# Optimization experiments

Hardware: AMD Instinct MI355X
Metric: run time of the kernel (lower is better)

Reference implementation:

```python
import jax, jax.numpy as jnp
import numpy as np

NUM_HEADS = 16
NEG_INF = -9e15


def setup_inputs() -> dict:
    key = jax.random.key(0)
    k1, k2, k3 = jax.random.split(key, 3)
    B, S, D = 2, 2048, 1024
    # xavier-uniform-ish init scale for weights
    lim_qkv = float(np.sqrt(6.0 / (D + 3 * D)))
    lim_o = float(np.sqrt(6.0 / (D + D)))
    return {
        "x": jax.random.normal(k1, (B, S, D), dtype=jnp.float32),
        "w_qkv": jax.random.uniform(k2, (3 * D, D), minval=-lim_qkv, maxval=lim_qkv, dtype=jnp.float32),
        "b_qkv": jnp.zeros((3 * D,), dtype=jnp.float32),
        "w_o": jax.random.uniform(k3, (D, D), minval=-lim_o, maxval=lim_o, dtype=jnp.float32),
        "b_o": jnp.zeros((D,), dtype=jnp.float32),
    }


def reference(x, w_qkv, b_qkv, w_o, b_o):
    B, S, D = x.shape
    H = NUM_HEADS
    hd = D // H
    # qkv projection: [B,S,3D]
    qkv = x @ w_qkv.T + b_qkv
    # -> [B, H, S, 3*hd], then split
    qkv = qkv.reshape(B, S, H, 3 * hd).transpose(0, 2, 1, 3)
    q, k, v = jnp.split(qkv, 3, axis=-1)  # each [B,H,S,hd]
    scale = 1.0 / jnp.sqrt(jnp.asarray(hd, dtype=x.dtype))
    logits = jnp.einsum("bhqd,bhkd->bhqk", q, k) * scale
    attn = jax.nn.softmax(logits, axis=-1)
    vals = jnp.einsum("bhqk,bhkd->bhqd", attn, v)
    vals = vals.transpose(0, 2, 1, 3).reshape(B, S, D)
    return vals @ w_o.T + b_o
```

## Files before the change

kernel.cpp:

```cpp
#include <hip/hip_runtime.h>
#include <math.h>

#define NHEADS 16
#define HD 64

typedef __attribute__((ext_vector_type(8))) _Float16 half8;
typedef __attribute__((ext_vector_type(4))) _Float16 half4;
typedef __attribute__((ext_vector_type(4))) float f32x4;
typedef __attribute__((ext_vector_type(16))) float f32x16;
typedef __attribute__((ext_vector_type(4))) unsigned int u32x4;

__device__ inline void load_lds16(const void* g, void* l) {
    __builtin_amdgcn_global_load_lds(
        (const __attribute__((address_space(1))) unsigned int*)g,
        (__attribute__((address_space(3))) unsigned int*)l, 16, 0, 0);
}
__device__ inline void pl32swap(unsigned int& x, unsigned int& y) {
    asm volatile("v_permlane32_swap_b32 %0, %1" : "+v"(x), "+v"(y));
}

#define NX  4194304
#define NWQ 3145728
#define NWO 1048576
__global__ void cvt_all(const float* __restrict__ x, const float* __restrict__ wq,
                        const float* __restrict__ wo, _Float16* __restrict__ xf,
                        _Float16* __restrict__ wqf, _Float16* __restrict__ wof) {
    int i = (blockIdx.x * blockDim.x + threadIdx.x) * 8;
    const float* src; _Float16* dst; int off;
    if (i < NX)            { src = x;  dst = xf;  off = i; }
    else if (i < NX + NWQ) { src = wq; dst = wqf; off = i - NX; }
    else                   { src = wo; dst = wof; off = i - (NX + NWQ); }
    float4 a = *(const float4*)(src + off);
    float4 b = *(const float4*)(src + off + 4);
    half8 h;
    h[0] = (_Float16)a.x; h[1] = (_Float16)a.y; h[2] = (_Float16)a.z; h[3] = (_Float16)a.w;
    h[4] = (_Float16)b.x; h[5] = (_Float16)b.y; h[6] = (_Float16)b.z; h[7] = (_Float16)b.w;
    *(half8*)(dst + off) = h;
}

#define GEMM_CORE(K)                                                                   \
    __shared__ __align__(1024) unsigned char smem[16384];                              \
    const int tid = threadIdx.x;                                                       \
    const int l = tid & 63, w = tid >> 6;                                              \
    const int wr = w >> 1, wc = w & 1;                                                 \
    const int nwg = gridDim.x * gridDim.y;                                             \
    const int bid = blockIdx.y * gridDim.x + blockIdx.x;                               \
    const int swz = (bid & 7) * (nwg >> 3) + (bid >> 3);                               \
    const int m0 = (swz / gridDim.x) * 128, n0 = (swz % gridDim.x) * 128;              \
    const int srow = tid >> 2;                                                         \
    const int schunk = (tid & 3) ^ ((srow >> 1) & 3);                                  \
    const size_t gA0 = (size_t)(m0 + srow) * K + schunk * 8;                           \
    const size_t gA1 = gA0 + (size_t)64 * K;                                           \
    const size_t gB0 = (size_t)(n0 + srow) * K + schunk * 8;                           \
    const size_t gB1 = gB0 + (size_t)64 * K;                                           \
    unsigned char* ldsW = smem + w * 1024;                                             \
    const int col16 = l & 15, kc = l >> 4;                                             \
    const int ra0 = wr * 64 + col16;                                                   \
    const int offA = ra0 * 64 + ((kc ^ ((ra0 >> 1) & 3)) * 16);                        \
    const int rb0 = wc * 64 + col16;                                                   \
    const int offB = rb0 * 64 + ((kc ^ ((rb0 >> 1) & 3)) * 16);                        \
    f32x4 acc[4][4] = {};                                                              \
    for (int k0 = 0; k0 < K; k0 += 32) {                                               \
        load_lds16(A + gA0 + k0, ldsW + 0);                                            \
        load_lds16(A + gA1 + k0, ldsW + 4096);                                         \
        load_lds16(B + gB0 + k0, ldsW + 8192);                                         \
        load_lds16(B + gB1 + k0, ldsW + 12288);                                       \
        __syncthreads();                                                               \
        half8 af[4], bf[4];                                                            \
        _Pragma("unroll")                                                              \
        for (int m = 0; m < 4; ++m) af[m] = *(const half8*)(smem + offA + m * 1024);   \
        _Pragma("unroll")                                                              \
        for (int n = 0; n < 4; ++n) bf[n] = *(const half8*)(smem + 8192 + offB + n * 1024); \
        _Pragma("unroll")                                                              \
        for (int m = 0; m < 4; ++m)                                                    \
            _Pragma("unroll")                                                          \
            for (int n = 0; n < 4; ++n)                                                \
                acc[m][n] = __builtin_amdgcn_mfma_f32_16x16x32_f16(af[m], bf[n], acc[m][n], 0, 0, 0); \
        __syncthreads();                                                               \
    }

__global__ __launch_bounds__(256, 2) void gemm_o(
    const _Float16* __restrict__ A, const _Float16* __restrict__ B,
    const float* __restrict__ bias, float* __restrict__ C,
    int M, int N, int K) {
    GEMM_CORE(K)
    const int rowb = m0 + wr * 64 + (l >> 4) * 4;
    const int colb = n0 + wc * 64 + col16;
    float bv[4];
    #pragma unroll
    for (int n = 0; n < 4; ++n) bv[n] = bias[colb + n * 16];
    #pragma unroll
    for (int m = 0; m < 4; ++m)
        #pragma unroll
        for (int j = 0; j < 4; ++j) {
            float* crow = C + (size_t)(rowb + m * 16 + j) * N + colb;
            #pragma unroll
            for (int n = 0; n < 4; ++n) crow[n * 16] = acc[m][n][j] + bv[n];
        }
}

#define QSCALE 0.18033688f
__global__ __launch_bounds__(256, 2) void gemm_qkv(
    const _Float16* __restrict__ A, const _Float16* __restrict__ B,
    const float* __restrict__ bias,
    _Float16* __restrict__ Qf, _Float16* __restrict__ Kf,
    _Float16* __restrict__ VfT, int K) {
    GEMM_CORE(K)
    const int rowb = m0 + wr * 64 + (l >> 4) * 4;
    const int colb = n0 + wc * 64 + col16;
    #pragma unroll
    for (int n = 0; n < 4; ++n) {
        int col = colb + n * 16;
        int h = col / 192;
        int rem = col - h * 192;
        int part = rem >> 6, d = rem & 63;
        float bv = bias[col];
        #pragma unroll
        for (int m = 0; m < 4; ++m) {
            int r0 = rowb + m * 16;
            int b = r0 >> 11, s0r = r0 & 2047;
            int bh = b * 16 + h;
            if (part == 0) {
                #pragma unroll
                for (int j = 0; j < 4; ++j)
                    Qf[((size_t)bh * 2048 + s0r + j) * 64 + d] =
                        (_Float16)((acc[m][n][j] + bv) * QSCALE);
            } else if (part == 1) {
                #pragma unroll
                for (int j = 0; j < 4; ++j)
                    Kf[((size_t)bh * 2048 + s0r + j) * 64 + d] = (_Float16)(acc[m][n][j] + bv);
            } else {
                half4 pk;
                pk[0] = (_Float16)(acc[m][n][0] + bv);
                pk[1] = (_Float16)(acc[m][n][1] + bv);
                pk[2] = (_Float16)(acc[m][n][2] + bv);
                pk[3] = (_Float16)(acc[m][n][3] + bv);
                *(half4*)&VfT[((size_t)bh * 64 + d) * 2048 + s0r] = pk;
            }
        }
    }
}

__global__ __launch_bounds__(512, 2) void mfma_attn(
    const _Float16* __restrict__ Qf, const _Float16* __restrict__ Kf,
    const _Float16* __restrict__ VfT, _Float16* __restrict__ vals) {
    __shared__ __align__(1024) unsigned char smem[32768];
    const int tid = threadIdx.x;
    const int l = tid & 63, w = tid >> 6;
    const int l31 = l & 31, hl = l >> 5;
    const int hwbid = blockIdx.y * gridDim.x + blockIdx.x;
    const int q_t = (hwbid >> 3) & 7;
    const int bh = (hwbid & 7) + ((hwbid >> 6) << 3);
    const int q0 = q_t * 256;
    const int h = bh & 15, b = bh >> 4;

    half8 qf[4];
    {
        const _Float16* qp = Qf + ((size_t)bh * 2048 + q0 + w * 32 + l31) * 64 + hl * 8;
        #pragma unroll
        for (int c = 0; c < 4; ++c) qf[c] = *(const half8*)(qp + c * 16);
    }
    f32x16 zvec = {};
    f32x16 o0 = {}, o1 = {};
    float mshift = 0.f, lsum = 0.f;

    const _Float16* Kg = Kf + (size_t)bh * 2048 * 64;
    const _Float16* Vg = VfT + (size_t)bh * 64 * 2048;

    int offK, offV;
    {
        int row2 = w * 4 + (l >> 4);
        int slot = (l & 15) ^ (row2 & 15);
        int row = row2 * 2 + (slot >> 3);
        int chunk = slot & 7;
        offK = row * 64 + chunk * 8;
        offV = row * 2048 + chunk * 8;
    }
    const int sbase = (l31 & 1) * 8;
    const int xr = (l31 >> 1) & 15;
    const int rb0 = (l31 >> 1) * 256;

    #define STAGE(kt0, buf)                                                            \
        {                                                                              \
            unsigned char* bK = smem + (buf) * 8192 + w * 1024;                        \
            unsigned char* bV = smem + 16384 + (buf) * 8192 + w * 1024;                \
            load_lds16(Kg + (size_t)(kt0) * 64 + offK, bK);                            \
            load_lds16(Vg + (kt0) + offV, bV);                                         \
        }

    STAGE(0, 0)
    __syncthreads();
    int cur = 0;
    for (int t = 0; t < 32; ++t) {
        if (t + 1 < 32) STAGE((t + 1) * 64, cur ^ 1)
        const unsigned char* Ksb = smem + cur * 8192;
        const unsigned char* Vsb = smem + 16384 + cur * 8192;

        f32x16 s0_, s1_;
        __builtin_amdgcn_s_setprio(1);
        {
            int chOff = ((sbase + hl) ^ xr) << 4;
            half8 k0 = *(const half8*)(Ksb + rb0 + chOff);
            half8 k1 = *(const half8*)(Ksb + rb0 + 4096 + chOff);
            s0_ = __builtin_amdgcn_mfma_f32_32x32x16_f16(k0, qf[0], zvec, 0, 0, 0);
            s1_ = __builtin_amdgcn_mfma_f32_32x32x16_f16(k1, qf[0], zvec, 0, 0, 0);
        }
        #pragma unroll
        for (int kc = 1; kc < 4; ++kc) {
            int chOff = ((sbase + kc * 2 + hl) ^ xr) << 4;
            half8 k0 = *(const half8*)(Ksb + rb0 + chOff);
            half8 k1 = *(const half8*)(Ksb + rb0 + 4096 + chOff);
            s0_ = __builtin_amdgcn_mfma_f32_32x32x16_f16(k0, qf[kc], s0_, 0, 0, 0);
            s1_ = __builtin_amdgcn_mfma_f32_32x32x16_f16(k1, qf[kc], s1_, 0, 0, 0);
        }
        __builtin_amdgcn_s_setprio(0);

        if (__any(mshift != 0.f)) {
            #pragma unroll
            for (int r = 0; r < 16; ++r) { s0_[r] -= mshift; s1_[r] -= mshift; }
        }

        float r0 = 0.f, r1 = 0.f, r2 = 0.f, r3 = 0.f;
        unsigned int a[2][8];
        #pragma unroll
        for (int j = 0; j < 8; ++j) {
            float p0 = __builtin_amdgcn_exp2f(s0_[2 * j]);
            float p1 = __builtin_amdgcn_exp2f(s0_[2 * j + 1]);
            float q0_ = __builtin_amdgcn_exp2f(s1_[2 * j]);
            float q1_ = __builtin_amdgcn_exp2f(s1_[2 * j + 1]);
            r0 += p0; r1 += p1; r2 += q0_; r3 += q1_;
            a[0][j] = __builtin_bit_cast(unsigned int, __builtin_amdgcn_cvt_pkrtz(p0, p1));
            a[1][j] = __builtin_bit_cast(unsigned int, __builtin_amdgcn_cvt_pkrtz(q0_, q1_));
        }
        float rsum = (r0 + r1) + (r2 + r3);

        if (__any(rsum > 32768.f)) {
            float pmax = s0_[0];
            #pragma unroll
            for (int r = 1; r < 16; ++r) pmax = fmaxf(pmax, s0_[r]);
            #pragma unroll
            for (int r = 0; r < 16; ++r) pmax = fmaxf(pmax, s1_[r]);
            pmax = fmaxf(pmax, __shfl_xor(pmax, 32, 64));
            float d_ = fmaxf(pmax, 0.f);
            float corr = __builtin_amdgcn_exp2f(-d_);
            #pragma unroll
            for (int r = 0; r < 16; ++r) { s0_[r] -= d_; s1_[r] -= d_; }
            #pragma unroll
            for (int r = 0; r < 16; ++r) { o0[r] *= corr; o1[r] *= corr; }
            lsum *= corr;
            mshift += d_;
            r0 = r1 = r2 = r3 = 0.f;
            #pragma unroll
            for (int j = 0; j < 8; ++j) {
                float p0 = __builtin_amdgcn_exp2f(s0_[2 * j]);
                float p1 = __builtin_amdgcn_exp2f(s0_[2 * j + 1]);
                float q0_ = __builtin_amdgcn_exp2f(s1_[2 * j]);
                float q1_ = __builtin_amdgcn_exp2f(s1_[2 * j + 1]);
                r0 += p0; r1 += p1; r2 += q0_; r3 += q1_;
                a[0][j] = __builtin_bit_cast(unsigned int, __builtin_amdgcn_cvt_pkrtz(p0, p1));
                a[1][j] = __builtin_bit_cast(unsigned int, __builtin_amdgcn_cvt_pkrtz(q0_, q1_));
            }
            rsum = (r0 + r1) + (r2 + r3);
        }
        lsum += rsum;

        #pragma unroll
        for (int c = 0; c < 2; ++c) {
            pl32swap(a[c][0], a[c][2]);
            pl32swap(a[c][1], a[c][3]);
            pl32swap(a[c][4], a[c][6]);
            pl32swap(a[c][5], a[c][7]);
        }

        __builtin_amdgcn_s_setprio(1);
        #pragma unroll
        for (int kk = 0; kk < 4; ++kk) {
            u32x4 pw;
            pw.x = a[kk >> 1][(kk & 1) * 4 + 0];
            pw.y = a[kk >> 1][(kk & 1) * 4 + 1];
            pw.z = a[kk >> 1][(kk & 1) * 4 + 2];
            pw.w = a[kk >> 1][(kk & 1) * 4 + 3];
            half8 pf = __builtin_bit_cast(half8, pw);
            int chOff = ((sbase + kk * 2 + hl) ^ xr) << 4;
            half8 v0 = *(const half8*)(Vsb + rb0 + chOff);
            half8 v1 = *(const half8*)(Vsb + rb0 + 4096 + chOff);
            o0 = __builtin_amdgcn_mfma_f32_32x32x16_f16(v0, pf, o0, 0, 0, 0);
            o1 = __builtin_amdgcn_mfma_f32_32x32x16_f16(v1, pf, o1, 0, 0, 0);
        }
        __builtin_amdgcn_s_setprio(0);
        __syncthreads();
        cur ^= 1;
    }

    lsum += __shfl_xor(lsum, 32, 64);
    float inv = 1.f / lsum;
    size_t orow = ((size_t)(b * 2048 + q0 + w * 32 + l31)) * 1024 + h * 64;
    #pragma unroll
    for (int dc = 0; dc < 2; ++dc) {
        const f32x16* op = dc ? &o1 : &o0;
        #pragma unroll
        for (int rq = 0; rq < 4; ++rq) {
            int d0 = dc * 32 + rq * 8 + hl * 4;
            half4 hv;
            #pragma unroll
            for (int j = 0; j < 4; ++j) hv[j] = (_Float16)((*op)[rq * 4 + j] * inv);
            *(half4*)(vals + orow + d0) = hv;
        }
    }
}

extern "C" void kernel_launch(void* const* d_in, const int* in_sizes, int n_in,
                              void* d_out, int out_size, void* d_ws, size_t ws_size,
                              hipStream_t stream) {
    const float* x     = (const float*)d_in[0];
    const float* w_qkv = (const float*)d_in[1];
    const float* b_qkv = (const float*)d_in[2];
    const float* w_o   = (const float*)d_in[3];
    const float* b_o   = (const float*)d_in[4];
    float* out = (float*)d_out;

    const int B = 2, S = 2048, D = 1024;
    const int M = B * S;
    const int N1 = 3 * D;
    const int BH = B * NHEADS;

    _Float16* xf  = (_Float16*)d_ws;
    _Float16* wqf = xf  + (size_t)M * D;
    _Float16* wof = wqf + (size_t)N1 * D;
    _Float16* Qf  = wof + (size_t)D * D;
    _Float16* Kf  = Qf  + (size_t)BH * S * HD;
    _Float16* VfT = Kf  + (size_t)BH * S * HD;
    _Float16* vals = xf;

    cvt_all<<<(NX + NWQ + NWO) / 2048, 256, 0, stream>>>(x, w_qkv, w_o, xf, wqf, wof);

    gemm_qkv<<<dim3(N1 / 128, M / 128), 256, 0, stream>>>(xf, wqf, b_qkv, Qf, Kf, VfT, D);

    mfma_attn<<<dim3(S / 256, BH), 512, 0, stream>>>(Qf, Kf, VfT, vals);

    gemm_o<<<dim3(D / 128, M / 128), 256, 0, stream>>>(vals, wof, b_o, out, M, D, D);
}
```

Before: 114.3 us.

## Software-pipeline attention loop: overlap next QK^T with current softmax and PV

Restructures the attention main loop so the QK^T MFMAs for tile t are issued before the softmax and PV of tile t-1. V now uses a triple buffer while K stays double-buffered, and the loop is unrolled by two with ping-pong score registers. The aim is to hide exp/softmax VALU latency behind matrix-core work. In exchange it raises LDS use to 40KB and register pressure from the extra live score tile, which could hurt occupancy at two blocks of 512 threads.

```diff
diff --git a/kernel.cpp b/kernel.cpp
--- a/kernel.cpp
+++ b/kernel.cpp
@@ -144,7 +144,7 @@
 __global__ __launch_bounds__(512, 2) void mfma_attn(
     const _Float16* __restrict__ Qf, const _Float16* __restrict__ Kf,
     const _Float16* __restrict__ VfT, _Float16* __restrict__ vals) {
-    __shared__ __align__(1024) unsigned char smem[32768];
+    __shared__ __align__(1024) unsigned char smem[40960];
     const int tid = threadIdx.x;
     const int l = tid & 63, w = tid >> 6;
     const int l31 = l & 31, hl = l >> 5;
@@ -180,117 +180,132 @@
     const int xr = (l31 >> 1) & 15;
     const int rb0 = (l31 >> 1) * 256;
 
-    #define STAGE(kt0, buf)                                                            \
+    #define STAGE(kt0, kbuf, vbuf)                                                     \
         {                                                                              \
-            unsigned char* bK = smem + (buf) * 8192 + w * 1024;                        \
-            unsigned char* bV = smem + 16384 + (buf) * 8192 + w * 1024;                \
+            unsigned char* bK = smem + (kbuf) * 8192 + w * 1024;                       \
+            unsigned char* bV = smem + 16384 + (vbuf) * 8192 + w * 1024;               \
             load_lds16(Kg + (size_t)(kt0) * 64 + offK, bK);                            \
             load_lds16(Vg + (kt0) + offV, bV);                                         \
         }
 
-    STAGE(0, 0)
+    #define QK_TILE(kb, D0, D1)                                                        \
+        {                                                                              \
+            const unsigned char* Ksb_ = smem + (kb) * 8192;                            \
+            __builtin_amdgcn_s_setprio(1);                                             \
+            {                                                                          \
+                int chOff = ((sbase + hl) ^ xr) << 4;                                  \
+                half8 k0_ = *(const half8*)(Ksb_ + rb0 + chOff);                       \
+                half8 k1_ = *(const half8*)(Ksb_ + rb0 + 4096 + chOff);                \
+                D0 = __builtin_amdgcn_mfma_f32_32x32x16_f16(k0_, qf[0], zvec, 0, 0, 0);\
+                D1 = __builtin_amdgcn_mfma_f32_32x32x16_f16(k1_, qf[0], zvec, 0, 0, 0);\
+            }                                                                          \
+            _Pragma("unroll")                                                          \
+            for (int kc = 1; kc < 4; ++kc) {                                           \
+                int chOff = ((sbase + kc * 2 + hl) ^ xr) << 4;                         \
+                half8 k0_ = *(const half8*)(Ksb_ + rb0 + chOff);                       \
+                half8 k1_ = *(const half8*)(Ksb_ + rb0 + 4096 + chOff);                \
+                D0 = __builtin_amdgcn_mfma_f32_32x32x16_f16(k0_, qf[kc], D0, 0, 0, 0); \
+                D1 = __builtin_amdgcn_mfma_f32_32x32x16_f16(k1_, qf[kc], D1, 0, 0, 0); \
+            }                                                                          \
+            __builtin_amdgcn_s_setprio(0);                                             \
+        }
+
+    #define SMPV(S0, S1)                                                               \
+        {                                                                              \
+            const unsigned char* Vsb_ = smem + 16384 + vrd * 8192;                     \
+            if (__any(mshift != 0.f)) {                                                \
+                _Pragma("unroll")                                                      \
+                for (int r = 0; r < 16; ++r) { S0[r] -= mshift; S1[r] -= mshift; }     \
+            }                                                                          \
+            float r0 = 0.f, r1 = 0.f, r2 = 0.f, r3 = 0.f;                              \
+            unsigned int a[2][8];                                                      \
+            _Pragma("unroll")                                                          \
+            for (int j = 0; j < 8; ++j) {                                              \
+                float p0 = __builtin_amdgcn_exp2f(S0[2 * j]);                          \
+                float p1 = __builtin_amdgcn_exp2f(S0[2 * j + 1]);                      \
+                float q0_ = __builtin_amdgcn_exp2f(S1[2 * j]);                         \
+                float q1_ = __builtin_amdgcn_exp2f(S1[2 * j + 1]);                     \
+                r0 += p0; r1 += p1; r2 += q0_; r3 += q1_;                              \
+                a[0][j] = __builtin_bit_cast(unsigned int, __builtin_amdgcn_cvt_pkrtz(p0, p1));   \
+                a[1][j] = __builtin_bit_cast(unsigned int, __builtin_amdgcn_cvt_pkrtz(q0_, q1_)); \
+            }                                                                          \
+            float rsum = (r0 + r1) + (r2 + r3);                                        \
+            if (__any(rsum > 32768.f)) {                                               \
+                float pmax = S0[0];                                                    \
+                _Pragma("unroll")                                                      \
+                for (int r = 1; r < 16; ++r) pmax = fmaxf(pmax, S0[r]);                \
+                _Pragma("unroll")                                                      \
+                for (int r = 0; r < 16; ++r) pmax = fmaxf(pmax, S1[r]);                \
+                pmax = fmaxf(pmax, __shfl_xor(pmax, 32, 64));                          \
+                float d_ = fmaxf(pmax, 0.f);                                           \
+                float corr = __builtin_amdgcn_exp2f(-d_);                              \
+                _Pragma("unroll")                                                      \
+                for (int r = 0; r < 16; ++r) { S0[r] -= d_; S1[r] -= d_; }             \
+                _Pragma("unroll")                                                      \
+                for (int r = 0; r < 16; ++r) { o0[r] *= corr; o1[r] *= corr; }         \
+                lsum *= corr;                                                          \
+                mshift += d_;                                                          \
+                r0 = r1 = r2 = r3 = 0.f;                                               \
+                _Pragma("unroll")                                                      \
+                for (int j = 0; j < 8; ++j) {                                          \
+                    float p0 = __builtin_amdgcn_exp2f(S0[2 * j]);                      \
+                    float p1 = __builtin_amdgcn_exp2f(S0[2 * j + 1]);                  \
+                    float q0_ = __builtin_amdgcn_exp2f(S1[2 * j]);                     \
+                    float q1_ = __builtin_amdgcn_exp2f(S1[2 * j + 1]);                 \
+                    r0 += p0; r1 += p1; r2 += q0_; r3 += q1_;                          \
+                    a[0][j] = __builtin_bit_cast(unsigned int, __builtin_amdgcn_cvt_pkrtz(p0, p1));   \
+                    a[1][j] = __builtin_bit_cast(unsigned int, __builtin_amdgcn_cvt_pkrtz(q0_, q1_)); \
+                }                                                                      \
+                rsum = (r0 + r1) + (r2 + r3);                                          \
+            }                                                                          \
+            lsum += rsum;                                                              \
+            _Pragma("unroll")                                                          \
+            for (int c = 0; c < 2; ++c) {                                              \
+                pl32swap(a[c][0], a[c][2]);                                            \
+                pl32swap(a[c][1], a[c][3]);                                            \
+                pl32swap(a[c][4], a[c][6]);                                            \
+                pl32swap(a[c][5], a[c][7]);                                            \
+            }                                                                          \
+            __builtin_amdgcn_s_setprio(1);                                             \
+            _Pragma("unroll")                                                          \
+            for (int kk = 0; kk < 4; ++kk) {                                           \
+                u32x4 pw;                                                              \
+                pw.x = a[kk >> 1][(kk & 1) * 4 + 0];                                   \
+                pw.y = a[kk >> 1][(kk & 1) * 4 + 1];                                   \
+                pw.z = a[kk >> 1][(kk & 1) * 4 + 2];                                   \
+                pw.w = a[kk >> 1][(kk & 1) * 4 + 3];                                   \
+                half8 pf = __builtin_bit_cast(half8, pw);                              \
+                int chOff = ((sbase + kk * 2 + hl) ^ xr) << 4;                         \
+                half8 v0 = *(const half8*)(Vsb_ + rb0 + chOff);                        \
+                half8 v1 = *(const half8*)(Vsb_ + rb0 + 4096 + chOff);                 \
+                o0 = __builtin_amdgcn_mfma_f32_32x32x16_f16(v0, pf, o0, 0, 0, 0);      \
+                o1 = __builtin_amdgcn_mfma_f32_32x32x16_f16(v1, pf, o1, 0, 0, 0);      \
+            }                                                                          \
+            __builtin_amdgcn_s_setprio(0);                                             \
+        }
+
+    #define ITER(tt, kb, D0, D1, P0, P1, dostage)                                      \
+        __syncthreads();                                                               \
+        if (dostage) STAGE(((tt) + 1) * 64, (kb) ^ 1, vst)                             \
+        QK_TILE(kb, D0, D1)                                                            \
+        SMPV(P0, P1)                                                                   \
+        vrd = (vrd == 2) ? 0 : vrd + 1;                                                \
+        vst = (vst == 2) ? 0 : vst + 1;
+
+    int vrd = 0, vst = 2;
+    f32x16 sA0, sA1, sB0, sB1;
+
+    STAGE(0, 0, 0)
     __syncthreads();
-    int cur = 0;
-    for (int t = 0; t < 32; ++t) {
-        if (t + 1 < 32) STAGE((t + 1) * 64, cur ^ 1)
-        const unsigned char* Ksb = smem + cur * 8192;
-        const unsigned char* Vsb = smem + 16384 + cur * 8192;
-
-        f32x16 s0_, s1_;
-        __builtin_amdgcn_s_setprio(1);
-        {
-            int chOff = ((sbase + hl) ^ xr) << 4;
-            half8 k0 = *(const half8*)(Ksb + rb0 + chOff);
-            half8 k1 = *(const half8*)(Ksb + rb0 + 4096 + chOff);
-            s0_ = __builtin_amdgcn_mfma_f32_32x32x16_f16(k0, qf[0], zvec, 0, 0, 0);
-            s1_ = __builtin_amdgcn_mfma_f32_32x32x16_f16(k1, qf[0], zvec, 0, 0, 0);
-        }
-        #pragma unroll
-        for (int kc = 1; kc < 4; ++kc) {
-            int chOff = ((sbase + kc * 2 + hl) ^ xr) << 4;
-            half8 k0 = *(const half8*)(Ksb + rb0 + chOff);
-            half8 k1 = *(const half8*)(Ksb + rb0 + 4096 + chOff);
-            s0_ = __builtin_amdgcn_mfma_f32_32x32x16_f16(k0, qf[kc], s0_, 0, 0, 0);
-            s1_ = __builtin_amdgcn_mfma_f32_32x32x16_f16(k1, qf[kc], s1_, 0, 0, 0);
-        }
-        __builtin_amdgcn_s_setprio(0);
-
-        if (__any(mshift != 0.f)) {
-            #pragma unroll
-            for (int r = 0; r < 16; ++r) { s0_[r] -= mshift; s1_[r] -= mshift; }
-        }
-
-        float r0 = 0.f, r1 = 0.f, r2 = 0.f, r3 = 0.f;
-        unsigned int a[2][8];
-        #pragma unroll
-        for (int j = 0; j < 8; ++j) {
-            float p0 = __builtin_amdgcn_exp2f(s0_[2 * j]);
-            float p1 = __builtin_amdgcn_exp2f(s0_[2 * j + 1]);
-            float q0_ = __builtin_amdgcn_exp2f(s1_[2 * j]);
-            float q1_ = __builtin_amdgcn_exp2f(s1_[2 * j + 1]);
-            r0 += p0; r1 += p1; r2 += q0_; r3 += q1_;
-            a[0][j] = __builtin_bit_cast(unsigned int, __builtin_amdgcn_cvt_pkrtz(p0, p1));
-            a[1][j] = __builtin_bit_cast(unsigned int, __builtin_amdgcn_cvt_pkrtz(q0_, q1_));
-        }
-        float rsum = (r0 + r1) + (r2 + r3);
-
-        if (__any(rsum > 32768.f)) {
-            float pmax = s0_[0];
-            #pragma unroll
-            for (int r = 1; r < 16; ++r) pmax = fmaxf(pmax, s0_[r]);
-            #pragma unroll
-            for (int r = 0; r < 16; ++r) pmax = fmaxf(pmax, s1_[r]);
-            pmax = fmaxf(pmax, __shfl_xor(pmax, 32, 64));
-            float d_ = fmaxf(pmax, 0.f);
-            float corr = __builtin_amdgcn_exp2f(-d_);
-            #pragma unroll
-            for (int r = 0; r < 16; ++r) { s0_[r] -= d_; s1_[r] -= d_; }
-            #pragma unroll
-            for (int r = 0; r < 16; ++r) { o0[r] *= corr; o1[r] *= corr; }
-            lsum *= corr;
-            mshift += d_;
-            r0 = r1 = r2 = r3 = 0.f;
-            #pragma unroll
-            for (int j = 0; j < 8; ++j) {
-                float p0 = __builtin_amdgcn_exp2f(s0_[2 * j]);
-                float p1 = __builtin_amdgcn_exp2f(s0_[2 * j + 1]);
-                float q0_ = __builtin_amdgcn_exp2f(s1_[2 * j]);
-                float q1_ = __builtin_amdgcn_exp2f(s1_[2 * j + 1]);
-                r0 += p0; r1 += p1; r2 += q0_; r3 += q1_;
-                a[0][j] = __builtin_bit_cast(unsigned int, __builtin_amdgcn_cvt_pkrtz(p0, p1));
-                a[1][j] = __builtin_bit_cast(unsigned int, __builtin_amdgcn_cvt_pkrtz(q0_, q1_));
-            }
-            rsum = (r0 + r1) + (r2 + r3);
-        }
-        lsum += rsum;
-
-        #pragma unroll
-        for (int c = 0; c < 2; ++c) {
-            pl32swap(a[c][0], a[c][2]);
-            pl32swap(a[c][1], a[c][3]);
-            pl32swap(a[c][4], a[c][6]);
-            pl32swap(a[c][5], a[c][7]);
-        }
-
-        __builtin_amdgcn_s_setprio(1);
-        #pragma unroll
-        for (int kk = 0; kk < 4; ++kk) {
-            u32x4 pw;
-            pw.x = a[kk >> 1][(kk & 1) * 4 + 0];
-            pw.y = a[kk >> 1][(kk & 1) * 4 + 1];
-            pw.z = a[kk >> 1][(kk & 1) * 4 + 2];
-            pw.w = a[kk >> 1][(kk & 1) * 4 + 3];
-            half8 pf = __builtin_bit_cast(half8, pw);
-            int chOff = ((sbase + kk * 2 + hl) ^ xr) << 4;
-            half8 v0 = *(const half8*)(Vsb + rb0 + chOff);
-            half8 v1 = *(const half8*)(Vsb + rb0 + 4096 + chOff);
-            o0 = __builtin_amdgcn_mfma_f32_32x32x16_f16(v0, pf, o0, 0, 0, 0);
-            o1 = __builtin_amdgcn_mfma_f32_32x32x16_f16(v1, pf, o1, 0, 0, 0);
-        }
-        __builtin_amdgcn_s_setprio(0);
-        __syncthreads();
-        cur ^= 1;
-    }
+    QK_TILE(0, sA0, sA1)
+    STAGE(64, 1, 1)
+
+    for (int t = 1; t < 31; t += 2) {
+        ITER(t, 1, sB0, sB1, sA0, sA1, 1)
+        ITER(t + 1, 0, sA0, sA1, sB0, sB1, 1)
+    }
+    ITER(31, 1, sB0, sB1, sA0, sA1, 0)
+    SMPV(sB0, sB1)
 
     lsum += __shfl_xor(lsum, 32, 64);
     float inv = 1.f / lsum;
```

New measurement: 112.9 us. No clear change (-1.2%).
